# Kernel optimization log

Measured on AMD Instinct MI355X. Metric: run time of the kernel, lower is better.

Reference implementation:

```python
import jax, jax.numpy as jnp
import numpy as np

N_USERS = 4096
N_ITEMS = 4096
D = 64  # embedding_dim / out_features
N = N_USERS + N_ITEMS
ALPHA = 0.2  # LeakyReLU slope
NEG_INF = jnp.float32(-9e15)


def setup_inputs() -> dict:
    key = jax.random.key(0)
    ks = jax.random.split(key, 11)
    s = 0.05  # xavier-ish scale
    rn = lambda k, shape: jax.random.normal(k, shape, jnp.float32) * s
    adj = jax.random.randint(ks[0], (N, N), 0, 2, jnp.int32)
    return {
        "adj": adj,
        "user_emb": rn(ks[1], (N_USERS, D)),
        "item_emb": rn(ks[2], (N_ITEMS, D)),
        "W0_w": rn(ks[3], (D, D)), "W0_b": rn(ks[4], (D,)), "a0": rn(ks[5], (2 * D, 1)),
        "W1_w": rn(ks[6], (D, D)), "W1_b": rn(ks[7], (D,)), "a1": rn(ks[8], (2 * D, 1)),
        "out_w": rn(ks[9], (D, D)), "out_b": rn(ks[10], (D,)),
    }


def gat_layer(x, adj, W_w, W_b, a):
    # Wh: [N, D]
    Wh = x @ W_w.T + W_b
    # Original materializes [N,N,2D] concat then matmul with a.
    # Algebraically identical: e_ij = leakyrelu(a1 . Wh_i + a2 . Wh_j)
    src = Wh @ a[:D]          # [N, 1] -> row contribution
    dst = (Wh @ a[D:]).T      # [1, N] -> column contribution
    e = jax.nn.leaky_relu(src + dst, ALPHA)        # [N, N]
    e = jnp.where(adj > 0, e, NEG_INF)
    att = jax.nn.softmax(e, axis=1)                # dropout=0.0 (eval)
    return att @ Wh                                 # [N, D]


def reference(adj, user_emb, item_emb, W0_w, W0_b, a0, W1_w, W1_b, a1, out_w, out_b):
    x = jnp.concatenate([user_emb, item_emb], axis=0)  # [N, D]
    x = jax.nn.relu(gat_layer(x, adj, W0_w, W0_b, a0))
    x = jax.nn.relu(gat_layer(x, adj, W1_w, W1_b, a1))
    u, it = x[:N_USERS], x[N_USERS:]
    return (u @ out_w.T + out_b, it @ out_w.T + out_b)
```

## Files before the change

kernel.cpp:

```cpp
#include <hip/hip_runtime.h>
#include <hip/hip_bf16.h>


typedef __attribute__((ext_vector_type(8))) __bf16 bf16x8;
typedef __attribute__((ext_vector_type(4))) float  f32x4;

union Frag {
    bf16x8         v;
    unsigned int   w[4];
    unsigned short h[8];
};

union BF2 {
    __hip_bfloat162 b;
    unsigned int    u;
};

__device__ __forceinline__ unsigned short f2bf(float f) {
    unsigned int u = __float_as_uint(f);
    u += 0x7FFFu + ((u >> 16) & 1u);
    return (unsigned short)(u >> 16);
}

__global__ __launch_bounds__(256) void k_pack(
    const int* __restrict__ adj, unsigned long long* __restrict__ bits)
{
    int wgid = blockIdx.x * 4 + (threadIdx.x >> 6);
    int lane = threadIdx.x & 63;
    const long long NW  = 2048LL * 4;
    const long long TOT = 8192LL * 8192;
    for (long long base = (long long)wgid * 512; base < TOT; base += NW * 512) {
        int a[8];
#pragma unroll
        for (int i = 0; i < 8; i++) a[i] = adj[base + i * 64 + lane];
        unsigned long long m[8];
#pragma unroll
        for (int i = 0; i < 8; i++) m[i] = __ballot(a[i] != 0);
        if (lane < 4) {
            reinterpret_cast<ulonglong2*>(bits + (base >> 6))[lane] =
                ulonglong2{m[2 * lane], m[2 * lane + 1]};
        }
    }
}

__device__ __forceinline__ void prep_tail(
    float (*xs)[65], float (*Wt)[65], float (*sred)[64], float (*dred)[64],
    const float* __restrict__ W, const float* __restrict__ bias,
    const float* __restrict__ avec,
    unsigned short* __restrict__ WhT,
    float* __restrict__ sraw, float* __restrict__ draw,
    float* __restrict__ E1, float* __restrict__ E2,
    float* __restrict__ F1, float* __restrict__ F2,
    int tid, int r0)
{
    for (int e = tid; e < 4096; e += 256) {
        int o = e >> 6, c = e & 63;
        Wt[c][o] = W[e];
    }
    __syncthreads();

    int r = tid & 63, chunk = tid >> 6, c0 = chunk * 16;
    float acc[16];
#pragma unroll
    for (int o = 0; o < 16; o++) acc[o] = bias[c0 + o];
    for (int c = 0; c < 64; c++) {
        float xv = xs[r][c];
#pragma unroll
        for (int o = 0; o < 16; o++) acc[o] += xv * Wt[c][c0 + o];
    }

    float sp = 0.f, dp = 0.f;
#pragma unroll
    for (int o = 0; o < 16; o++) {
        sp += acc[o] * avec[c0 + o];
        dp += acc[o] * avec[64 + c0 + o];
    }
    sred[chunk][r] = sp;
    dred[chunk][r] = dp;

#pragma unroll
    for (int o = 0; o < 16; o++)
        WhT[(c0 + o) * 8192 + r0 + r] = f2bf(acc[o]);

    __syncthreads();
    if (tid < 64) {
        int g = r0 + tid;
        float s = sred[0][tid] + sred[1][tid] + sred[2][tid] + sred[3][tid];
        float d = dred[0][tid] + dred[1][tid] + dred[2][tid] + dred[3][tid];
        sraw[g] = s;  E1[g] = __expf(s);  E2[g] = __expf(0.2f * s);
        draw[g] = d;  F1[g] = __expf(d);  F2[g] = __expf(0.2f * d);
    }
}

__global__ __launch_bounds__(256) void k_prep0(
    const float* __restrict__ ue, const float* __restrict__ ie,
    const float* __restrict__ W, const float* __restrict__ bias,
    const float* __restrict__ avec,
    unsigned short* __restrict__ WhT,
    float* __restrict__ sraw, float* __restrict__ draw,
    float* __restrict__ E1, float* __restrict__ E2,
    float* __restrict__ F1, float* __restrict__ F2)
{
    __shared__ float xs[64][65];
    __shared__ float Wt[64][65];
    __shared__ float sred[4][64];
    __shared__ float dred[4][64];
    int tid = threadIdx.x, r0 = blockIdx.x * 64;

    for (int e = tid; e < 4096; e += 256) {
        int r = e >> 6, c = e & 63;
        int row = r0 + r;
        xs[r][c] = (row < 4096) ? ue[row * 64 + c] : ie[(row - 4096) * 64 + c];
    }
    prep_tail(xs, Wt, sred, dred, W, bias, avec, WhT, sraw, draw,
              E1, E2, F1, F2, tid, r0);
}

template <int NS>
__global__ __launch_bounds__(256) void k_prep1(
    const float* __restrict__ numP, const float* __restrict__ denP,
    const float* __restrict__ W, const float* __restrict__ bias,
    const float* __restrict__ avec,
    unsigned short* __restrict__ WhT,
    float* __restrict__ sraw, float* __restrict__ draw,
    float* __restrict__ E1, float* __restrict__ E2,
    float* __restrict__ F1, float* __restrict__ F2)
{
    __shared__ float xs[64][65];
    __shared__ float Wt[64][65];
    __shared__ float sred[4][64];
    __shared__ float dred[4][64];
    __shared__ float dtot[64];
    int tid = threadIdx.x, r0 = blockIdx.x * 64;
    int rowblk = blockIdx.x;

    if (tid < 64) {
        float s = 0.f;
#pragma unroll
        for (int p = 0; p < NS; p++) s += denP[p * 8192 + r0 + tid];
        dtot[tid] = fmaxf(s, 1e-20f);
    }
    __syncthreads();
    for (int e = tid; e < 4096; e += 256) {
        int r = e >> 6;
        float s = 0.f;
#pragma unroll
        for (int p = 0; p < NS; p++)
            s += numP[(size_t)(p * 128 + rowblk) * 4096 + e];
        float v = s / dtot[r];
        xs[r][e & 63] = v > 0.f ? v : 0.f;
    }
    prep_tail(xs, Wt, sred, dred, W, bias, avec, WhT, sraw, draw,
              E1, E2, F1, F2, tid, r0);
}

struct AggSmem {
    union {
        unsigned short WhB[64][264];
        struct {
            float T[64][68];
            float denT[64];
        } ep;
    } u;
    float dvL[256], f1L[256], f2L[256];
    unsigned int mkL[64][8];
};

__device__ __forceinline__ void agg_body(
    const unsigned int* __restrict__ bits32,
    const unsigned short* __restrict__ WhT,
    const float* __restrict__ sraw,
    const float* __restrict__ E1v, const float* __restrict__ E2v,
    const float* __restrict__ draw,
    const float* __restrict__ F1v, const float* __restrict__ F2v,
    float* __restrict__ numP, float* __restrict__ denP)
{
    constexpr int KR = 256;
    __shared__ AggSmem sm;

    int tid  = threadIdx.x;
    int wave = tid >> 6, lane = tid & 63;
    int quad = lane >> 4, l16 = lane & 15;
    int rowblk = blockIdx.x, ks = blockIdx.y;
    int k0  = ks * KR;

    for (int p = tid; p < 64 * 32; p += 256) {
        int f = p >> 5, c8 = (p & 31) * 8;
        *reinterpret_cast<uint4*>(&sm.u.WhB[f][c8]) =
            *reinterpret_cast<const uint4*>(WhT + (size_t)f * 8192 + k0 + c8);
    }
    if (tid < 256) {
        sm.dvL[tid] = draw[k0 + tid];
        sm.f1L[tid] = F1v[k0 + tid];
        sm.f2L[tid] = F2v[k0 + tid];
    }
    for (int p = tid; p < 512; p += 256)
        sm.mkL[p >> 3][p & 7] =
            bits32[(rowblk * 64 + (p >> 3)) * 256 + ks * 8 + (p & 7)];
    __syncthreads();

    int row = rowblk * 64 + wave * 16 + l16;
    float sv = sraw[row], e1 = E1v[row], e2 = E2v[row];

    f32x4 accs[4];
    f32x4 accd = {0.f, 0.f, 0.f, 0.f};
#pragma unroll
    for (int nt = 0; nt < 4; nt++) accs[nt] = accd;

    Frag ones;
    ones.w[0] = ones.w[1] = ones.w[2] = ones.w[3] = 0x3F803F80u;

    int lrow = wave * 16 + l16;
#pragma unroll 2
    for (int kb = 0; kb < KR; kb += 32) {
        int kq = kb + quad * 8;

        unsigned int mask8 = (sm.mkL[lrow][kb >> 5] >> (quad * 8)) & 0xFFu;
        float4 dd0 = *reinterpret_cast<const float4*>(&sm.dvL[kq]);
        float4 dd1 = *reinterpret_cast<const float4*>(&sm.dvL[kq + 4]);
        float4 fa0 = *reinterpret_cast<const float4*>(&sm.f1L[kq]);
        float4 fa1 = *reinterpret_cast<const float4*>(&sm.f1L[kq + 4]);
        float4 fb0 = *reinterpret_cast<const float4*>(&sm.f2L[kq]);
        float4 fb1 = *reinterpret_cast<const float4*>(&sm.f2L[kq + 4]);
        float dva[8] = {dd0.x, dd0.y, dd0.z, dd0.w, dd1.x, dd1.y, dd1.z, dd1.w};
        float f1a[8] = {fa0.x, fa0.y, fa0.z, fa0.w, fa1.x, fa1.y, fa1.z, fa1.w};
        float f2a[8] = {fb0.x, fb0.y, fb0.z, fb0.w, fb1.x, fb1.y, fb1.z, fb1.w};

        Frag A;
#pragma unroll
        for (int p = 0; p < 4; p++) {
            float w2[2];
#pragma unroll
            for (int h = 0; h < 2; h++) {
                int j = 2 * p + h;
                float t   = sv + dva[j];
                bool  neg = t < 0.f;
                float ww  = (neg ? e2 : e1) * (neg ? f2a[j] : f1a[j]);
                w2[h] = ((mask8 >> j) & 1u) ? ww : 0.f;
            }
            BF2 cv;
            cv.b = __float22bfloat162_rn(float2{w2[0], w2[1]});
            A.w[p] = cv.u;
        }

#pragma unroll
        for (int nt = 0; nt < 4; nt++) {
            Frag B;
            B.v = *reinterpret_cast<const bf16x8*>(&sm.u.WhB[nt * 16 + l16][kq]);
            accs[nt] = __builtin_amdgcn_mfma_f32_16x16x32_bf16(A.v, B.v,
                                                               accs[nt], 0, 0, 0);
        }
        accd = __builtin_amdgcn_mfma_f32_16x16x32_bf16(A.v, ones.v, accd, 0, 0, 0);
    }

    __syncthreads();
#pragma unroll
    for (int rr = 0; rr < 4; rr++) {
        int r = wave * 16 + quad * 4 + rr;
#pragma unroll
        for (int nt = 0; nt < 4; nt++)
            sm.u.ep.T[r][nt * 16 + l16] = accs[nt][rr];
        if (l16 == 0) sm.u.ep.denT[r] = accd[rr];
    }
    __syncthreads();

    float* dst = numP + (size_t)(ks * 128 + rowblk) * 4096;
#pragma unroll
    for (int i = 0; i < 4; i++) {
        int idx = i * 1024 + tid * 4;
        int r = idx >> 6, c = idx & 63;
        float4 v = *reinterpret_cast<const float4*>(&sm.u.ep.T[r][c]);
        *reinterpret_cast<float4*>(dst + idx) = v;
    }
    if (tid < 64)
        denP[ks * 8192 + rowblk * 64 + tid] = sm.u.ep.denT[tid];
}

__global__ __launch_bounds__(256) void k_agg_l0(
    const unsigned int* __restrict__ bits32, const unsigned short* __restrict__ WhT,
    const float* __restrict__ sraw,
    const float* __restrict__ E1v, const float* __restrict__ E2v,
    const float* __restrict__ draw,
    const float* __restrict__ F1v, const float* __restrict__ F2v,
    float* __restrict__ numP, float* __restrict__ denP)
{
    agg_body(bits32, WhT, sraw, E1v, E2v, draw, F1v, F2v, numP, denP);
}

__global__ __launch_bounds__(256) void k_agg_l1(
    const unsigned int* __restrict__ bits32, const unsigned short* __restrict__ WhT,
    const float* __restrict__ sraw,
    const float* __restrict__ E1v, const float* __restrict__ E2v,
    const float* __restrict__ draw,
    const float* __restrict__ F1v, const float* __restrict__ F2v,
    float* __restrict__ numP, float* __restrict__ denP)
{
    agg_body(bits32, WhT, sraw, E1v, E2v, draw, F1v, F2v, numP, denP);
}

template <int NS>
__global__ __launch_bounds__(256) void k_out(
    const float* __restrict__ numP, const float* __restrict__ denP,
    const float* __restrict__ W, const float* __restrict__ bias,
    float* __restrict__ out)
{
    __shared__ float xs[64][65];
    __shared__ float Wt[64][65];
    __shared__ float dtot[64];
    int tid = threadIdx.x, r0 = blockIdx.x * 64;
    int rowblk = blockIdx.x;

    if (tid < 64) {
        float s = 0.f;
#pragma unroll
        for (int p = 0; p < NS; p++) s += denP[p * 8192 + r0 + tid];
        dtot[tid] = fmaxf(s, 1e-20f);
    }
    __syncthreads();
    for (int e = tid; e < 4096; e += 256) {
        int r = e >> 6;
        float s = 0.f;
#pragma unroll
        for (int p = 0; p < NS; p++)
            s += numP[(size_t)(p * 128 + rowblk) * 4096 + e];
        float v = s / dtot[r];
        xs[r][e & 63] = v > 0.f ? v : 0.f;
    }
    for (int e = tid; e < 4096; e += 256) {
        int o = e >> 6, c = e & 63;
        Wt[c][o] = W[e];
    }
    __syncthreads();

    int r = tid & 63, chunk = tid >> 6, c0 = chunk * 16;
    float acc[16];
#pragma unroll
    for (int o = 0; o < 16; o++) acc[o] = bias[c0 + o];
    for (int c = 0; c < 64; c++) {
        float xv = xs[r][c];
#pragma unroll
        for (int o = 0; o < 16; o++) acc[o] += xv * Wt[c][c0 + o];
    }
#pragma unroll
    for (int o = 0; o < 16; o++)
        out[(r0 + r) * 64 + c0 + o] = acc[o];
}

extern "C" void kernel_launch(void* const* d_in, const int* in_sizes, int n_in,
                              void* d_out, int out_size, void* d_ws, size_t ws_size,
                              hipStream_t stream)
{
    const int*   adj = (const int*)d_in[0];
    const float* ue  = (const float*)d_in[1];
    const float* ie  = (const float*)d_in[2];
    const float* W0w = (const float*)d_in[3];
    const float* W0b = (const float*)d_in[4];
    const float* a0  = (const float*)d_in[5];
    const float* W1w = (const float*)d_in[6];
    const float* W1b = (const float*)d_in[7];
    const float* a1  = (const float*)d_in[8];
    const float* Ow  = (const float*)d_in[9];
    const float* Ob  = (const float*)d_in[10];

    constexpr int NS = 32;

    char* ws = (char*)d_ws;
    size_t off = 0;
    auto alloc = [&](size_t bytes) -> char* {
        char* p = ws + off;
        off += (bytes + 255) & ~(size_t)255;
        return p;
    };
    float*          numP    = (float*)alloc((size_t)NS * 524288 * 4);
    float*          denP    = (float*)alloc((size_t)NS * 8192 * 4);
    unsigned long long* adjbits = (unsigned long long*)alloc(8192 * 1024);
    unsigned short* WhT0    = (unsigned short*)alloc(64 * 8192 * 2);
    unsigned short* WhT1    = (unsigned short*)alloc(64 * 8192 * 2);
    float* sr0 = (float*)alloc(8192 * 4); float* dr0 = (float*)alloc(8192 * 4);
    float* E10 = (float*)alloc(8192 * 4); float* E20 = (float*)alloc(8192 * 4);
    float* F10 = (float*)alloc(8192 * 4); float* F20 = (float*)alloc(8192 * 4);
    float* sr1 = (float*)alloc(8192 * 4); float* dr1 = (float*)alloc(8192 * 4);
    float* E11 = (float*)alloc(8192 * 4); float* E21 = (float*)alloc(8192 * 4);
    float* F11 = (float*)alloc(8192 * 4); float* F21 = (float*)alloc(8192 * 4);

    const unsigned int* bits32 = (const unsigned int*)adjbits;

    k_pack<<<2048, 256, 0, stream>>>(adj, adjbits);

    k_prep0<<<128, 256, 0, stream>>>(ue, ie, W0w, W0b, a0, WhT0,
                                     sr0, dr0, E10, E20, F10, F20);
    k_agg_l0<<<dim3(128, NS), 256, 0, stream>>>(bits32, WhT0, sr0, E10, E20,
                                                dr0, F10, F20, numP, denP);
    k_prep1<NS><<<128, 256, 0, stream>>>(numP, denP, W1w, W1b, a1, WhT1,
                                         sr1, dr1, E11, E21, F11, F21);
    k_agg_l1<<<dim3(128, NS), 256, 0, stream>>>(bits32, WhT1, sr1, E11, E21,
                                                dr1, F11, F21, numP, denP);
    k_out<NS><<<128, 256, 0, stream>>>(numP, denP, Ow, Ob, (float*)d_out);
}
```

Before: 538.6 us.

## Process four K-chunks per block with register-prefetched double buffering, fewer splits

Each aggregation block now walks four 256-wide K chunks instead of one. While it computes on the current chunk, it prefetches the next chunk's Wh tile, the dst/F vectors and the mask words into registers, then stores them to shared memory between barriers. The split count NS drops from 32 to 8, which shrinks the partial numerator/denominator buffers and the reduction traffic, but there are fewer blocks (128x8). Holding the prefetch in registers raises register pressure and may lower occupancy.

```diff
diff --git a/kernel.cpp b/kernel.cpp
--- a/kernel.cpp
+++ b/kernel.cpp
@@ -166,6 +166,52 @@
     unsigned int mkL[64][8];
 };
 
+struct Pref {
+    uint4 w[8];
+    float dv, f1, f2;
+    unsigned int mk[2];
+};
+
+__device__ __forceinline__ void pref_load(
+    Pref& P, int tid, int rowblk, int kc,
+    const unsigned short* __restrict__ WhT,
+    const float* __restrict__ draw,
+    const float* __restrict__ F1v, const float* __restrict__ F2v,
+    const unsigned int* __restrict__ bits32)
+{
+#pragma unroll
+    for (int i = 0; i < 8; i++) {
+        int p = tid + 256 * i, f = p >> 5, c8 = (p & 31) * 8;
+        P.w[i] = *reinterpret_cast<const uint4*>(WhT + (size_t)f * 8192 + kc + c8);
+    }
+    P.dv = draw[kc + tid];
+    P.f1 = F1v[kc + tid];
+    P.f2 = F2v[kc + tid];
+    int kw = kc >> 5;
+#pragma unroll
+    for (int j = 0; j < 2; j++) {
+        int p = tid + 256 * j;
+        P.mk[j] = bits32[(rowblk * 64 + (p >> 3)) * 256 + kw + (p & 7)];
+    }
+}
+
+__device__ __forceinline__ void pref_store(const Pref& P, AggSmem& sm, int tid)
+{
+#pragma unroll
+    for (int i = 0; i < 8; i++) {
+        int p = tid + 256 * i, f = p >> 5, c8 = (p & 31) * 8;
+        *reinterpret_cast<uint4*>(&sm.u.WhB[f][c8]) = P.w[i];
+    }
+    sm.dvL[tid] = P.dv;
+    sm.f1L[tid] = P.f1;
+    sm.f2L[tid] = P.f2;
+#pragma unroll
+    for (int j = 0; j < 2; j++) {
+        int p = tid + 256 * j;
+        sm.mkL[p >> 3][p & 7] = P.mk[j];
+    }
+}
+
 __device__ __forceinline__ void agg_body(
     const unsigned int* __restrict__ bits32,
     const unsigned short* __restrict__ WhT,
@@ -175,28 +221,18 @@
     const float* __restrict__ F1v, const float* __restrict__ F2v,
     float* __restrict__ numP, float* __restrict__ denP)
 {
-    constexpr int KR = 256;
+    constexpr int CK = 256, NCH = 4;
     __shared__ AggSmem sm;
 
     int tid  = threadIdx.x;
     int wave = tid >> 6, lane = tid & 63;
     int quad = lane >> 4, l16 = lane & 15;
     int rowblk = blockIdx.x, ks = blockIdx.y;
-    int k0  = ks * KR;
-
-    for (int p = tid; p < 64 * 32; p += 256) {
-        int f = p >> 5, c8 = (p & 31) * 8;
-        *reinterpret_cast<uint4*>(&sm.u.WhB[f][c8]) =
-            *reinterpret_cast<const uint4*>(WhT + (size_t)f * 8192 + k0 + c8);
-    }
-    if (tid < 256) {
-        sm.dvL[tid] = draw[k0 + tid];
-        sm.f1L[tid] = F1v[k0 + tid];
-        sm.f2L[tid] = F2v[k0 + tid];
-    }
-    for (int p = tid; p < 512; p += 256)
-        sm.mkL[p >> 3][p & 7] =
-            bits32[(rowblk * 64 + (p >> 3)) * 256 + ks * 8 + (p & 7)];
+    int k0  = ks * (CK * NCH);
+
+    Pref P;
+    pref_load(P, tid, rowblk, k0, WhT, draw, F1v, F2v, bits32);
+    pref_store(P, sm, tid);
     __syncthreads();
 
     int row = rowblk * 64 + wave * 16 + l16;
@@ -211,46 +247,59 @@
     ones.w[0] = ones.w[1] = ones.w[2] = ones.w[3] = 0x3F803F80u;
 
     int lrow = wave * 16 + l16;
+
+    for (int c = 0; c < NCH; c++) {
+        if (c + 1 < NCH)
+            pref_load(P, tid, rowblk, k0 + (c + 1) * CK,
+                      WhT, draw, F1v, F2v, bits32);
+
 #pragma unroll 2
-    for (int kb = 0; kb < KR; kb += 32) {
-        int kq = kb + quad * 8;
-
-        unsigned int mask8 = (sm.mkL[lrow][kb >> 5] >> (quad * 8)) & 0xFFu;
-        float4 dd0 = *reinterpret_cast<const float4*>(&sm.dvL[kq]);
-        float4 dd1 = *reinterpret_cast<const float4*>(&sm.dvL[kq + 4]);
-        float4 fa0 = *reinterpret_cast<const float4*>(&sm.f1L[kq]);
-        float4 fa1 = *reinterpret_cast<const float4*>(&sm.f1L[kq + 4]);
-        float4 fb0 = *reinterpret_cast<const float4*>(&sm.f2L[kq]);
-        float4 fb1 = *reinterpret_cast<const float4*>(&sm.f2L[kq + 4]);
-        float dva[8] = {dd0.x, dd0.y, dd0.z, dd0.w, dd1.x, dd1.y, dd1.z, dd1.w};
-        float f1a[8] = {fa0.x, fa0.y, fa0.z, fa0.w, fa1.x, fa1.y, fa1.z, fa1.w};
-        float f2a[8] = {fb0.x, fb0.y, fb0.z, fb0.w, fb1.x, fb1.y, fb1.z, fb1.w};
-
-        Frag A;
-#pragma unroll
-        for (int p = 0; p < 4; p++) {
-            float w2[2];
-#pragma unroll
-            for (int h = 0; h < 2; h++) {
-                int j = 2 * p + h;
-                float t   = sv + dva[j];
-                bool  neg = t < 0.f;
-                float ww  = (neg ? e2 : e1) * (neg ? f2a[j] : f1a[j]);
-                w2[h] = ((mask8 >> j) & 1u) ? ww : 0.f;
+        for (int kb = 0; kb < CK; kb += 32) {
+            int kq = kb + quad * 8;
+
+            unsigned int mask8 = (sm.mkL[lrow][kb >> 5] >> (quad * 8)) & 0xFFu;
+            float4 dd0 = *reinterpret_cast<const float4*>(&sm.dvL[kq]);
+            float4 dd1 = *reinterpret_cast<const float4*>(&sm.dvL[kq + 4]);
+            float4 fa0 = *reinterpret_cast<const float4*>(&sm.f1L[kq]);
+            float4 fa1 = *reinterpret_cast<const float4*>(&sm.f1L[kq + 4]);
+            float4 fb0 = *reinterpret_cast<const float4*>(&sm.f2L[kq]);
+            float4 fb1 = *reinterpret_cast<const float4*>(&sm.f2L[kq + 4]);
+            float dva[8] = {dd0.x, dd0.y, dd0.z, dd0.w, dd1.x, dd1.y, dd1.z, dd1.w};
+            float f1a[8] = {fa0.x, fa0.y, fa0.z, fa0.w, fa1.x, fa1.y, fa1.z, fa1.w};
+            float f2a[8] = {fb0.x, fb0.y, fb0.z, fb0.w, fb1.x, fb1.y, fb1.z, fb1.w};
+
+            Frag A;
+#pragma unroll
+            for (int p = 0; p < 4; p++) {
+                float w2[2];
+#pragma unroll
+                for (int h = 0; h < 2; h++) {
+                    int j = 2 * p + h;
+                    float t   = sv + dva[j];
+                    bool  neg = t < 0.f;
+                    float ww  = (neg ? e2 : e1) * (neg ? f2a[j] : f1a[j]);
+                    w2[h] = ((mask8 >> j) & 1u) ? ww : 0.f;
+                }
+                BF2 cv;
+                cv.b = __float22bfloat162_rn(float2{w2[0], w2[1]});
+                A.w[p] = cv.u;
             }
-            BF2 cv;
-            cv.b = __float22bfloat162_rn(float2{w2[0], w2[1]});
-            A.w[p] = cv.u;
+
+#pragma unroll
+            for (int nt = 0; nt < 4; nt++) {
+                Frag B;
+                B.v = *reinterpret_cast<const bf16x8*>(&sm.u.WhB[nt * 16 + l16][kq]);
+                accs[nt] = __builtin_amdgcn_mfma_f32_16x16x32_bf16(A.v, B.v,
+                                                                   accs[nt], 0, 0, 0);
+            }
+            accd = __builtin_amdgcn_mfma_f32_16x16x32_bf16(A.v, ones.v, accd, 0, 0, 0);
         }
 
-#pragma unroll
-        for (int nt = 0; nt < 4; nt++) {
-            Frag B;
-            B.v = *reinterpret_cast<const bf16x8*>(&sm.u.WhB[nt * 16 + l16][kq]);
-            accs[nt] = __builtin_amdgcn_mfma_f32_16x16x32_bf16(A.v, B.v,
-                                                               accs[nt], 0, 0, 0);
+        if (c + 1 < NCH) {
+            __syncthreads();
+            pref_store(P, sm, tid);
+            __syncthreads();
         }
-        accd = __builtin_amdgcn_mfma_f32_16x16x32_bf16(A.v, ones.v, accd, 0, 0, 0);
     }
 
     __syncthreads();
@@ -268,8 +317,8 @@
 #pragma unroll
     for (int i = 0; i < 4; i++) {
         int idx = i * 1024 + tid * 4;
-        int r = idx >> 6, c = idx & 63;
-        float4 v = *reinterpret_cast<const float4*>(&sm.u.ep.T[r][c]);
+        int r = idx >> 6, c2 = idx & 63;
+        float4 v = *reinterpret_cast<const float4*>(&sm.u.ep.T[r][c2]);
         *reinterpret_cast<float4*>(dst + idx) = v;
     }
     if (tid < 64)
@@ -362,7 +411,7 @@
     const float* Ow  = (const float*)d_in[9];
     const float* Ob  = (const float*)d_in[10];
 
-    constexpr int NS = 32;
+    constexpr int NS = 8;
 
     char* ws = (char*)d_ws;
     size_t off = 0;
```

Result: no change. 543.8 us (+1.0%).
